# Optimization experiments

Measured on AMD Instinct MI355X. Metric: run time of the kernel, lower is better.

The kernel has to match this reference:

```python
import jax, jax.numpy as jnp
import numpy as np
from jax import lax

DIM = 256
QK = 256
HEADS = 8
NWIN = 7
TOPK = 4
KS = 5
SCALE = QK ** (-0.5)


def setup_inputs() -> dict:
    key = jax.random.key(0)
    ks = jax.random.split(key, 5)
    N, H, W = 8, 56, 56
    x = jax.random.normal(ks[0], (N, H, W, DIM), jnp.float32)
    W_qkv = jax.random.normal(ks[1], (DIM, QK + QK + DIM), jnp.float32) * 0.02
    b_qkv = jnp.zeros((QK + QK + DIM,), jnp.float32)
    lepe_w = jax.random.normal(ks[2], (DIM, 1, KS, KS), jnp.float32) * 0.05  # OIHW depthwise
    lepe_b = jnp.zeros((DIM,), jnp.float32)
    W_o = jax.random.normal(ks[3], (DIM, DIM), jnp.float32) * 0.02
    b_o = jnp.zeros((DIM,), jnp.float32)
    return {"x": x, "W_qkv": W_qkv, "b_qkv": b_qkv, "lepe_w": lepe_w,
            "lepe_b": lepe_b, "W_o": W_o, "b_o": b_o}


def reference(x, W_qkv, b_qkv, lepe_w, lepe_b, W_o, b_o):
    N, H, Wd, C = x.shape
    j = i = NWIN
    h, w = H // j, Wd // i
    p2, w2 = j * i, h * w
    hd, hdv = QK // HEADS, DIM // HEADS

    # window partition: n (j h) (i w) c -> n (j i) h w c
    xw = x.reshape(N, j, h, i, w, C).transpose(0, 1, 3, 2, 4, 5).reshape(N, p2, h, w, C)

    qkv = xw @ W_qkv + b_qkv                       # [N, p2, h, w, 2*QK+DIM... actually QK+(QK+DIM)]
    q = qkv[..., :QK]                              # [N, p2, h, w, QK]
    kv = qkv[..., QK:]                             # [N, p2, h, w, QK+DIM]

    q_pix = q.reshape(N, p2, w2, QK)
    kv_pix = kv.reshape(N, p2, w2, QK + DIM)       # identity kv_down

    q_win = q.mean(axis=(2, 3))                    # [N, p2, QK]
    k_win = kv[..., :QK].mean(axis=(2, 3))         # [N, p2, QK]

    # LePE: depthwise conv on v, in image layout
    v_img = kv[..., QK:].reshape(N, j, i, h, w, DIM).transpose(0, 5, 1, 3, 2, 4).reshape(N, DIM, H, Wd)
    pad = KS // 2
    lepe = lax.conv_general_dilated(v_img, lepe_w, (1, 1), [(pad, pad), (pad, pad)],
                                    feature_group_count=DIM)
    lepe = lepe + lepe_b[None, :, None, None]
    lepe = lepe.transpose(0, 2, 3, 1)              # [N, H, W, DIM]

    # coarse routing (detached in original when diff_routing=False)
    qd = lax.stop_gradient(q_win)
    kd = lax.stop_gradient(k_win)
    logit = jnp.einsum('npc,nqc->npq', qd * SCALE, kd)   # [N, p2, p2]
    _, r_idx = lax.top_k(logit, TOPK)              # [N, p2, TOPK]

    # gather top-k windows of kv (mul_weight='none')
    nidx = jnp.arange(N)[:, None, None]
    kv_sel = kv_pix[nidx, r_idx]                   # [N, p2, TOPK, w2, QK+DIM]
    k_sel = kv_sel[..., :QK].reshape(N, p2, TOPK * w2, HEADS, hd).transpose(0, 1, 3, 2, 4)
    v_sel = kv_sel[..., QK:].reshape(N, p2, TOPK * w2, HEADS, hdv).transpose(0, 1, 3, 2, 4)
    qh = q_pix.reshape(N, p2, w2, HEADS, hd).transpose(0, 1, 3, 2, 4)

    attn = jax.nn.softmax(jnp.einsum('npmwc,npmkc->npmwk', qh * SCALE, k_sel), axis=-1)
    out = jnp.einsum('npmwk,npmkc->npmwc', attn, v_sel)  # [N, p2, HEADS, w2, hdv]

    # back to image: (n p2) m (h w) c -> n (j h) (i w) (m c)
    out = out.transpose(0, 1, 3, 2, 4).reshape(N, j, i, h, w, DIM)
    out = out.transpose(0, 1, 3, 2, 4, 5).reshape(N, H, Wd, DIM)

    out = out + lepe
    out = out @ W_o + b_o
    return out
```

## Files before the change

### kernel.cpp

```cpp
#include <hip/hip_runtime.h>
#include <hip/hip_bf16.h>
#include <math.h>

#define NBATCH 8
#define HWDIM  56
#define NWIN   7
#define P2     49
#define HEADS  8
#define TOPK   4
#define SCALE  0.0625f
#define NPIX   (NBATCH*HWDIM*HWDIM)

typedef __attribute__((ext_vector_type(8))) short bf16x8;
typedef __attribute__((ext_vector_type(4))) float f32x4;

#define GLOBAL_AS __attribute__((address_space(1)))
#define LDS_AS    __attribute__((address_space(3)))

__device__ __forceinline__ void gload16(const unsigned short* g, unsigned short* l) {
  __builtin_amdgcn_global_load_lds((const GLOBAL_AS unsigned int*)g,
                                   (LDS_AS unsigned int*)l, 16, 0, 0);
}

__device__ __forceinline__ unsigned short f2bf(float f) {
  __hip_bfloat16 h = __float2bfloat16(f);
  return *reinterpret_cast<unsigned short*>(&h);
}
__device__ __forceinline__ float bf2f(unsigned short h) {
  return __uint_as_float(((unsigned)h) << 16);
}

__global__ __launch_bounds__(256) void conv_xwin(
    const float* __restrict__ x, unsigned short* __restrict__ xb,
    float* __restrict__ xw)
{
  __shared__ float4 red[256];
  const int bidx = blockIdx.x;
  const int n = bidx / P2, p = bidx - n * P2;
  const int y0 = (p / NWIN) * 8, x0 = (p % NWIN) * 8;
  const int t = threadIdx.x;
  const int c4 = t & 63, pg = t >> 6;
  float4 s = {0.f, 0.f, 0.f, 0.f};
  #pragma unroll
  for (int k = 0; k < 16; ++k) {
    const int pix = pg * 16 + k;
    const int yy = y0 + (pix >> 3), xx = x0 + (pix & 7);
    const size_t off = ((size_t)((n * HWDIM + yy) * HWDIM + xx)) * 256 + c4 * 4;
    float4 v = *(const float4*)&x[off];
    ushort4 o = { f2bf(v.x), f2bf(v.y), f2bf(v.z), f2bf(v.w) };
    *(ushort4*)&xb[off] = o;
    s.x += v.x; s.y += v.y; s.z += v.z; s.w += v.w;
  }
  red[t] = s;
  __syncthreads();
  if (pg == 0) {
    float4 a = red[c4], b = red[64 + c4], c = red[128 + c4], d = red[192 + c4];
    float4 o = { (a.x + b.x + c.x + d.x) * (1.f/64.f),
                 (a.y + b.y + c.y + d.y) * (1.f/64.f),
                 (a.z + b.z + c.z + d.z) * (1.f/64.f),
                 (a.w + b.w + c.w + d.w) * (1.f/64.f) };
    *(float4*)&xw[(size_t)bidx * 256 + c4 * 4] = o;
  }
}

__global__ __launch_bounds__(256) void prep_w(
    const float* __restrict__ W_qkv, const float* __restrict__ b_qkv,
    const float* __restrict__ W_o, const float* __restrict__ lepe_w,
    unsigned short* __restrict__ Wt_qkv, unsigned short* __restrict__ Wt_o,
    float* __restrict__ b_s, float* __restrict__ Wc)
{
  const int idx = blockIdx.x * 256 + threadIdx.x;
  if (idx < 768 * 256) {
    const int nn = idx >> 8, cc = idx & 255;
    float v = W_qkv[cc * 768 + nn];
    if (nn < 256) v *= SCALE;
    Wt_qkv[idx] = f2bf(v);
  } else if (idx < 768 * 256 + 256 * 256) {
    const int j = idx - 768 * 256;
    const int nn = j >> 8, cc = j & 255;
    Wt_o[j] = f2bf(W_o[cc * 256 + nn]);
  } else if (idx < 768 * 256 + 256 * 256 + 768) {
    const int j = idx - (768 * 256 + 256 * 256);
    b_s[j] = b_qkv[j] * (j < 256 ? SCALE : 1.f);
  } else if (idx < 768 * 256 + 256 * 256 + 768 + 25 * 256) {
    const int j = idx - (768 * 256 + 256 * 256 + 768);
    const int tap = j >> 8, cc = j & 255;
    Wc[j] = lepe_w[cc * 25 + tap];
  }
}

__global__ __launch_bounds__(256) void win_gemm(
    const float* __restrict__ xw, const float* __restrict__ W_qkv,
    const float* __restrict__ b_qkv,
    float* __restrict__ q_win, float* __restrict__ k_win)
{
  __shared__ float xs[256];
  const int bidx = blockIdx.x;
  const int t = threadIdx.x;
  xs[t] = xw[(size_t)bidx * 256 + t];
  __syncthreads();
  float aq = 0.f, ak = 0.f;
  for (int cc = 0; cc < 256; ++cc) {
    const float xv = xs[cc];
    aq = fmaf(xv, W_qkv[cc * 768 + t], aq);
    ak = fmaf(xv, W_qkv[cc * 768 + 256 + t], ak);
  }
  q_win[(size_t)bidx * 256 + t] = aq + b_qkv[t];
  k_win[(size_t)bidx * 256 + t] = ak + b_qkv[256 + t];
}

__global__ __launch_bounds__(256) void routing_topk(
    const float* __restrict__ q_win, const float* __restrict__ k_win,
    int* __restrict__ r_idx)
{
  __shared__ float qs[256];
  __shared__ float logit[64];
  const int bidx = blockIdx.x;
  const int n = bidx / P2;
  const int t = threadIdx.x;
  qs[t] = q_win[(size_t)bidx * 256 + t];
  __syncthreads();
  const int qq = t >> 2, qt = t & 3;
  if (qq < P2) {
    const float* kb = k_win + ((size_t)(n * P2 + qq)) * 256 + qt * 64;
    float a = 0.f;
    #pragma unroll 8
    for (int i = 0; i < 64; ++i) a = fmaf(qs[qt * 64 + i], kb[i], a);
    a += __shfl_xor(a, 1);
    a += __shfl_xor(a, 2);
    if (qt == 0) logit[qq] = a;
  }
  __syncthreads();
  if (t == 0) {
    float bv0 = -3e38f, bv1 = -3e38f, bv2 = -3e38f, bv3 = -3e38f;
    int bi0 = 0, bi1 = 0, bi2 = 0, bi3 = 0;
    for (int q2 = 0; q2 < P2; ++q2) {
      const float v = logit[q2];
      if (v > bv0) { bv3=bv2; bi3=bi2; bv2=bv1; bi2=bi1; bv1=bv0; bi1=bi0; bv0=v; bi0=q2; }
      else if (v > bv1) { bv3=bv2; bi3=bi2; bv2=bv1; bi2=bi1; bv1=v; bi1=q2; }
      else if (v > bv2) { bv3=bv2; bi3=bi2; bv2=v; bi2=q2; }
      else if (v > bv3) { bv3=v; bi3=q2; }
    }
    int* rp = r_idx + (size_t)bidx * TOPK;
    rp[0] = bi0; rp[1] = bi1; rp[2] = bi2; rp[3] = bi3;
  }
}

template<int MODE>
__global__ __launch_bounds__(512) void gemm_mfma(
    const unsigned short* __restrict__ A,
    const unsigned short* __restrict__ Bt,
    const float* __restrict__ bias,
    unsigned short* __restrict__ C0, unsigned short* __restrict__ C1,
    unsigned short* __restrict__ C2, float* __restrict__ Cf)
{
  __shared__ char smem[49152];
  unsigned short* Asm = (unsigned short*)smem;
  unsigned short* Bsm = (unsigned short*)(smem + 16384);
  float* Cs = (float*)smem;

  const int t = threadIdx.x;
  const int w = t >> 6, l = t & 63;
  const int wr = w >> 2, wc = w & 3;
  const int lr = l & 15, lg = l >> 4;
  const int bm = blockIdx.x, bn = blockIdx.y;
  const int row0 = bm * 128, col0 = bn * 256;

  const f32x4 fzero = {0.f, 0.f, 0.f, 0.f};
  f32x4 acc[4][4];
  #pragma unroll
  for (int m = 0; m < 4; ++m)
    #pragma unroll
    for (int n = 0; n < 4; ++n) acc[m][n] = fzero;

  const int srow  = t >> 3;
  const int skoff = ((t & 7) ^ (srow & 7)) * 8;

  for (int step = 0; step < 4; ++step) {
    const int k0 = step * 64;
    #pragma unroll
    for (int i = 0; i < 2; ++i)
      gload16(&A [(size_t)(row0 + i*64 + srow) * 256 + k0 + skoff],
              Asm + i*4096 + t*8);
    #pragma unroll
    for (int i = 0; i < 4; ++i)
      gload16(&Bt[(size_t)(col0 + i*64 + srow) * 256 + k0 + skoff],
              Bsm + i*4096 + t*8);
    __syncthreads();
    #pragma unroll
    for (int kk = 0; kk < 2; ++kk) {
      bf16x8 af[4], bb[4];
      #pragma unroll
      for (int m = 0; m < 4; ++m)
        af[m] = *(const bf16x8*)&Asm[(wr*64 + m*16 + lr) * 64 + ((kk*4 + lg) ^ (lr & 7)) * 8];
      #pragma unroll
      for (int n = 0; n < 4; ++n)
        bb[n] = *(const bf16x8*)&Bsm[(wc*64 + n*16 + lr) * 64 + ((kk*4 + lg) ^ (lr & 7)) * 8];
      #pragma unroll
      for (int m = 0; m < 4; ++m)
        #pragma unroll
        for (int n = 0; n < 4; ++n)
          acc[m][n] = __builtin_amdgcn_mfma_f32_16x16x32_bf16(af[m], bb[n], acc[m][n], 0, 0, 0);
    }
    __syncthreads();
  }

  float bcol[4];
  #pragma unroll
  for (int n = 0; n < 4; ++n) bcol[n] = bias[col0 + wc*64 + n*16 + lr];

  #pragma unroll
  for (int hf = 0; hf < 4; ++hf) {
    if (hf) __syncthreads();
    if (wr == (hf >> 1)) {
      const int mbase = (hf & 1) * 2;
      #pragma unroll
      for (int mm = 0; mm < 2; ++mm)
        #pragma unroll
        for (int n = 0; n < 4; ++n)
          #pragma unroll
          for (int r = 0; r < 4; ++r) {
            const int lrow = mm*16 + lg*4 + r;
            const int col  = wc*64 + n*16 + lr;
            const int csw  = col ^ ((lrow & 7) << 2);
            Cs[lrow * 256 + csw] = acc[mbase + mm][n][r] + bcol[n];
          }
    }
    __syncthreads();
    #pragma unroll
    for (int it = 0; it < 4; ++it) {
      const int d = (it * 512 + t) * 4;
      const int lrow = d >> 8;
      const int colL = (d & 255) ^ ((lrow & 7) << 2);
      f32x4 v = *(const f32x4*)&Cs[d];
      const size_t grow = (size_t)(row0 + hf*32 + lrow);
      if (MODE == 0) {
        unsigned short* Cp = (bn == 0) ? C0 : (bn == 1) ? C1 : C2;
        ushort4 o = { f2bf(v[0]), f2bf(v[1]), f2bf(v[2]), f2bf(v[3]) };
        *(ushort4*)&Cp[grow * 256 + colL] = o;
      } else {
        float4 o = { v[0], v[1], v[2], v[3] };
        *(float4*)&Cf[grow * 256 + colL] = o;
      }
    }
  }
}

#define PSTR 272

__global__ __launch_bounds__(256) void attn_mfma(
    const unsigned short* __restrict__ q_bf,
    const unsigned short* __restrict__ k_bf,
    const unsigned short* __restrict__ v_bf,
    const int* __restrict__ r_idx,
    unsigned short* __restrict__ o_bf)
{
  __shared__ char smem[52480];
  unsigned short* Ksm = (unsigned short*)smem;
  unsigned short* Qsm = (unsigned short*)(smem + 16384);
  unsigned short* Psm = (unsigned short*)smem;
  unsigned short* Vsm = (unsigned short*)(smem + 34816);
  float*          Osm = (float*)(smem + 34816);
  float*          Ls  = (float*)(smem + 52224);

  const int b = blockIdx.x;
  const int h = b & 7;
  const int np = b >> 3;
  const int n = np / P2, p = np - n * P2;
  const int t = threadIdx.x;
  const int w = t >> 6, l = t & 63;
  const int lr = l & 15, lg = l >> 4;

  const int4 rv = *(const int4*)&r_idx[np * 4];

  {
    const int pix = t >> 2, ch = t & 3;
    #pragma unroll
    for (int i = 0; i < 4; ++i) {
      const int wv = (&rv.x)[i];
      const int ky = (wv / NWIN) * 8 + (pix >> 3);
      const int kx = (wv % NWIN) * 8 + (pix & 7);
      const size_t goff = ((size_t)((n * HWDIM + ky) * HWDIM + kx)) * 256 + h * 32;
      gload16(&k_bf[goff + ch * 8], Ksm + i * 2048 + t * 8);
    }
    const int qy = (p / NWIN) * 8 + (pix >> 3);
    const int qx = (p % NWIN) * 8 + (pix & 7);
    gload16(&q_bf[((size_t)((n * HWDIM + qy) * HWDIM + qx)) * 256 + h * 32 + ch * 8],
            Qsm + t * 8);
  }
  {
    const int s = t >> 6, pix = t & 63;
    const int wv = (&rv.x)[s];
    const int ky = (wv / NWIN) * 8 + (pix >> 3);
    const int kx = (wv % NWIN) * 8 + (pix & 7);
    const size_t goff = ((size_t)((n * HWDIM + ky) * HWDIM + kx)) * 256 + h * 32;
    #pragma unroll
    for (int j = 0; j < 4; ++j) {
      bf16x8 vv = *(const bf16x8*)&v_bf[goff + j * 8];
      #pragma unroll
      for (int e = 0; e < 8; ++e)
        Vsm[(j * 8 + e) * PSTR + t] = (unsigned short)vv[e];
    }
  }
  __syncthreads();

  f32x4 sf[16];
  {
    const f32x4 fzero = {0.f, 0.f, 0.f, 0.f};
    bf16x8 aq = *(const bf16x8*)&Qsm[(w * 16 + lr) * 32 + lg * 8];
    #pragma unroll
    for (int f = 0; f < 16; ++f) {
      bf16x8 bk = *(const bf16x8*)&Ksm[(f * 16 + lr) * 32 + lg * 8];
      sf[f] = __builtin_amdgcn_mfma_f32_16x16x32_bf16(bk, aq, fzero, 0, 0, 0);
    }
  }

  {
    float mx = sf[0][0];
    #pragma unroll
    for (int f = 0; f < 16; ++f)
      #pragma unroll
      for (int r = 0; r < 4; ++r) mx = fmaxf(mx, sf[f][r]);
    mx = fmaxf(mx, __shfl_xor(mx, 16));
    mx = fmaxf(mx, __shfl_xor(mx, 32));
    float sum = 0.f;
    #pragma unroll
    for (int f = 0; f < 16; ++f)
      #pragma unroll
      for (int r = 0; r < 4; ++r) {
        float e = __expf(sf[f][r] - mx);
        sf[f][r] = e; sum += e;
      }
    sum += __shfl_xor(sum, 16);
    sum += __shfl_xor(sum, 32);
    if (lg == 0) Ls[w * 16 + lr] = 1.f / sum;
  }
  __syncthreads();

  #pragma unroll
  for (int f = 0; f < 16; ++f) {
    ushort4 pk = { f2bf(sf[f][0]), f2bf(sf[f][1]), f2bf(sf[f][2]), f2bf(sf[f][3]) };
    *(ushort4*)&Psm[(w * 16 + lr) * PSTR + f * 16 + lg * 4] = pk;
  }

  f32x4 oacc[2];
  oacc[0] = (f32x4){0.f, 0.f, 0.f, 0.f};
  oacc[1] = (f32x4){0.f, 0.f, 0.f, 0.f};
  #pragma unroll
  for (int ks = 0; ks < 8; ++ks) {
    bf16x8 ap = *(const bf16x8*)&Psm[(w * 16 + lr) * PSTR + ks * 32 + lg * 8];
    #pragma unroll
    for (int nn = 0; nn < 2; ++nn) {
      bf16x8 bv = *(const bf16x8*)&Vsm[(nn * 16 + lr) * PSTR + ks * 32 + lg * 8];
      oacc[nn] = __builtin_amdgcn_mfma_f32_16x16x32_bf16(ap, bv, oacc[nn], 0, 0, 0);
    }
  }

  float inv4[4];
  #pragma unroll
  for (int r = 0; r < 4; ++r) inv4[r] = Ls[w * 16 + lg * 4 + r];

  __syncthreads();
  #pragma unroll
  for (int nn = 0; nn < 2; ++nn)
    #pragma unroll
    for (int r = 0; r < 4; ++r)
      Osm[(w * 16 + lg * 4 + r) * 36 + nn * 16 + lr] = oacc[nn][r] * inv4[r];
  __syncthreads();
  {
    const int q = t >> 2, dq = (t & 3) * 8;
    const int qy = (p / NWIN) * 8 + (q >> 3);
    const int qx = (p % NWIN) * 8 + (q & 7);
    float vo[8];
    #pragma unroll
    for (int e = 0; e < 8; ++e) vo[e] = Osm[q * 36 + dq + e];
    ushort4 o0 = { f2bf(vo[0]), f2bf(vo[1]), f2bf(vo[2]), f2bf(vo[3]) };
    ushort4 o1 = { f2bf(vo[4]), f2bf(vo[5]), f2bf(vo[6]), f2bf(vo[7]) };
    unsigned short* op = &o_bf[((size_t)((n * HWDIM + qy) * HWDIM + qx)) * 256 + h * 32 + dq];
    *(ushort4*)op = o0;
    *(ushort4*)&op[4] = o1;
  }
}

__global__ __launch_bounds__(256) void lepe_add(
    const unsigned short* __restrict__ v_bf, const float* __restrict__ Wc,
    const float* __restrict__ bias, unsigned short* __restrict__ o_bf)
{
  const int gid = blockIdx.x * 256 + threadIdx.x;
  const int c8 = (gid & 31) * 8;
  const int pix = gid >> 5;
  const int n = pix / (HWDIM * HWDIM);
  const int rem = pix - n * (HWDIM * HWDIM);
  const int y = rem / HWDIM, x = rem - y * HWDIM;

  float acc[8];
  {
    float4 b0 = *(const float4*)&bias[c8];
    float4 b1 = *(const float4*)&bias[c8 + 4];
    acc[0]=b0.x; acc[1]=b0.y; acc[2]=b0.z; acc[3]=b0.w;
    acc[4]=b1.x; acc[5]=b1.y; acc[6]=b1.z; acc[7]=b1.w;
  }

  #pragma unroll
  for (int ky = 0; ky < 5; ++ky) {
    const int sy = y + ky - 2;
    if (sy < 0 || sy >= HWDIM) continue;
    #pragma unroll
    for (int kx = 0; kx < 5; ++kx) {
      const int sx = x + kx - 2;
      if (sx < 0 || sx >= HWDIM) continue;
      const bf16x8 vv = *(const bf16x8*)&v_bf[((size_t)((n * HWDIM + sy) * HWDIM + sx)) * 256 + c8];
      const float* wp = &Wc[(ky * 5 + kx) * 256 + c8];
      float4 w0 = *(const float4*)wp;
      float4 w1 = *(const float4*)(wp + 4);
      acc[0] = fmaf(w0.x, bf2f((unsigned short)vv[0]), acc[0]);
      acc[1] = fmaf(w0.y, bf2f((unsigned short)vv[1]), acc[1]);
      acc[2] = fmaf(w0.z, bf2f((unsigned short)vv[2]), acc[2]);
      acc[3] = fmaf(w0.w, bf2f((unsigned short)vv[3]), acc[3]);
      acc[4] = fmaf(w1.x, bf2f((unsigned short)vv[4]), acc[4]);
      acc[5] = fmaf(w1.y, bf2f((unsigned short)vv[5]), acc[5]);
      acc[6] = fmaf(w1.z, bf2f((unsigned short)vv[6]), acc[6]);
      acc[7] = fmaf(w1.w, bf2f((unsigned short)vv[7]), acc[7]);
    }
  }

  unsigned short* op = &o_bf[(size_t)pix * 256 + c8];
  const bf16x8 ov = *(const bf16x8*)op;
  ushort4 o0 = { f2bf(bf2f((unsigned short)ov[0]) + acc[0]),
                 f2bf(bf2f((unsigned short)ov[1]) + acc[1]),
                 f2bf(bf2f((unsigned short)ov[2]) + acc[2]),
                 f2bf(bf2f((unsigned short)ov[3]) + acc[3]) };
  ushort4 o1 = { f2bf(bf2f((unsigned short)ov[4]) + acc[4]),
                 f2bf(bf2f((unsigned short)ov[5]) + acc[5]),
                 f2bf(bf2f((unsigned short)ov[6]) + acc[6]),
                 f2bf(bf2f((unsigned short)ov[7]) + acc[7]) };
  *(ushort4*)op = o0;
  *(ushort4*)(op + 4) = o1;
}

extern "C" void kernel_launch(void* const* d_in, const int* in_sizes, int n_in,
                              void* d_out, int out_size, void* d_ws, size_t ws_size,
                              hipStream_t stream)
{
  const float* x      = (const float*)d_in[0];
  const float* W_qkv  = (const float*)d_in[1];
  const float* b_qkv  = (const float*)d_in[2];
  const float* lepe_w = (const float*)d_in[3];
  const float* lepe_b = (const float*)d_in[4];
  const float* W_o    = (const float*)d_in[5];
  const float* b_o    = (const float*)d_in[6];
  float* out = (float*)d_out;

  char* ws = (char*)d_ws;
  const size_t IMG = (size_t)NPIX * 256;
  unsigned short* x_bf    = (unsigned short*)(ws);
  unsigned short* q_bf    = (unsigned short*)(ws + 2*IMG);
  unsigned short* k_bf    = (unsigned short*)(ws + 4*IMG);
  unsigned short* v_bf    = (unsigned short*)(ws + 6*IMG);
  unsigned short* attn_bf = (unsigned short*)(ws + 8*IMG);
  unsigned short* Wt_qkv  = (unsigned short*)(ws + 10*IMG);
  unsigned short* Wt_o    = (unsigned short*)(ws + 10*IMG + 393216);
  float*          b_s     = (float*)         (ws + 10*IMG + 393216 + 131072);
  float*          x_win   = (float*)         (ws + 10*IMG + 393216 + 131072 + 4096);
  float*          q_win   = x_win + (size_t)NBATCH * P2 * 256;
  float*          k_win   = q_win + (size_t)NBATCH * P2 * 256;
  int*            ridx    = (int*)(k_win + (size_t)NBATCH * P2 * 256);
  float*          Wc      = (float*)(ridx + (size_t)NBATCH * P2 * TOPK);

  conv_xwin<<<NBATCH * P2, 256, 0, stream>>>(x, x_bf, x_win);
  prep_w<<<1052, 256, 0, stream>>>(W_qkv, b_qkv, W_o, lepe_w, Wt_qkv, Wt_o, b_s, Wc);
  win_gemm<<<NBATCH * P2, 256, 0, stream>>>(x_win, W_qkv, b_qkv, q_win, k_win);
  routing_topk<<<NBATCH * P2, 256, 0, stream>>>(q_win, k_win, ridx);
  gemm_mfma<0><<<dim3(196, 3), 512, 0, stream>>>(x_bf, Wt_qkv, b_s,
                                                 q_bf, k_bf, v_bf, nullptr);
  attn_mfma<<<NBATCH * P2 * HEADS, 256, 0, stream>>>(q_bf, k_bf, v_bf, ridx, attn_bf);
  lepe_add<<<3136, 256, 0, stream>>>(v_bf, Wc, lepe_b, attn_bf);
  gemm_mfma<1><<<dim3(196, 1), 512, 0, stream>>>(attn_bf, Wt_o, b_o,
                                                 nullptr, nullptr, nullptr, out);
}
```

Before: 217.4 us.

## Fuse preprocessing kernels, fold LePE conv into attention epilogue, add MFMA priority hints

Merges the bf16 conversion, window-mean, window q/k GEMM and weight-prep kernels into one launch with block-range dispatch. It also moves the depthwise LePE convolution into the attention kernel's epilogue, so the separate read-modify-write of the attention output is gone. s_setprio hints are wrapped around the MFMA loops in the GEMM and attention kernels. This removes launches and an extra pass over attn_bf, but makes the attention epilogue heavier with 25 strided v_bf loads per thread, which may hurt that kernel's occupancy or latency.

```diff
diff --git a/kernel.cpp b/kernel.cpp
--- a/kernel.cpp
+++ b/kernel.cpp
@@ -30,83 +30,74 @@
   return __uint_as_float(((unsigned)h) << 16);
 }
 
-__global__ __launch_bounds__(256) void conv_xwin(
-    const float* __restrict__ x, unsigned short* __restrict__ xb,
-    float* __restrict__ xw)
+__global__ __launch_bounds__(256) void fused_pre(
+    const float* __restrict__ x, const float* __restrict__ W_qkv,
+    const float* __restrict__ b_qkv, const float* __restrict__ W_o,
+    const float* __restrict__ lepe_w,
+    unsigned short* __restrict__ xb, float* __restrict__ q_win,
+    float* __restrict__ k_win, unsigned short* __restrict__ Wt_qkv,
+    unsigned short* __restrict__ Wt_o, float* __restrict__ b_s,
+    float* __restrict__ Wc)
 {
   __shared__ float4 red[256];
-  const int bidx = blockIdx.x;
-  const int n = bidx / P2, p = bidx - n * P2;
-  const int y0 = (p / NWIN) * 8, x0 = (p % NWIN) * 8;
-  const int t = threadIdx.x;
-  const int c4 = t & 63, pg = t >> 6;
-  float4 s = {0.f, 0.f, 0.f, 0.f};
-  #pragma unroll
-  for (int k = 0; k < 16; ++k) {
-    const int pix = pg * 16 + k;
-    const int yy = y0 + (pix >> 3), xx = x0 + (pix & 7);
-    const size_t off = ((size_t)((n * HWDIM + yy) * HWDIM + xx)) * 256 + c4 * 4;
-    float4 v = *(const float4*)&x[off];
-    ushort4 o = { f2bf(v.x), f2bf(v.y), f2bf(v.z), f2bf(v.w) };
-    *(ushort4*)&xb[off] = o;
-    s.x += v.x; s.y += v.y; s.z += v.z; s.w += v.w;
-  }
-  red[t] = s;
-  __syncthreads();
-  if (pg == 0) {
-    float4 a = red[c4], b = red[64 + c4], c = red[128 + c4], d = red[192 + c4];
-    float4 o = { (a.x + b.x + c.x + d.x) * (1.f/64.f),
-                 (a.y + b.y + c.y + d.y) * (1.f/64.f),
-                 (a.z + b.z + c.z + d.z) * (1.f/64.f),
-                 (a.w + b.w + c.w + d.w) * (1.f/64.f) };
-    *(float4*)&xw[(size_t)bidx * 256 + c4 * 4] = o;
-  }
-}
-
-__global__ __launch_bounds__(256) void prep_w(
-    const float* __restrict__ W_qkv, const float* __restrict__ b_qkv,
-    const float* __restrict__ W_o, const float* __restrict__ lepe_w,
-    unsigned short* __restrict__ Wt_qkv, unsigned short* __restrict__ Wt_o,
-    float* __restrict__ b_s, float* __restrict__ Wc)
-{
-  const int idx = blockIdx.x * 256 + threadIdx.x;
-  if (idx < 768 * 256) {
-    const int nn = idx >> 8, cc = idx & 255;
-    float v = W_qkv[cc * 768 + nn];
-    if (nn < 256) v *= SCALE;
-    Wt_qkv[idx] = f2bf(v);
-  } else if (idx < 768 * 256 + 256 * 256) {
-    const int j = idx - 768 * 256;
-    const int nn = j >> 8, cc = j & 255;
-    Wt_o[j] = f2bf(W_o[cc * 256 + nn]);
-  } else if (idx < 768 * 256 + 256 * 256 + 768) {
-    const int j = idx - (768 * 256 + 256 * 256);
-    b_s[j] = b_qkv[j] * (j < 256 ? SCALE : 1.f);
-  } else if (idx < 768 * 256 + 256 * 256 + 768 + 25 * 256) {
-    const int j = idx - (768 * 256 + 256 * 256 + 768);
-    const int tap = j >> 8, cc = j & 255;
-    Wc[j] = lepe_w[cc * 25 + tap];
-  }
-}
-
-__global__ __launch_bounds__(256) void win_gemm(
-    const float* __restrict__ xw, const float* __restrict__ W_qkv,
-    const float* __restrict__ b_qkv,
-    float* __restrict__ q_win, float* __restrict__ k_win)
-{
   __shared__ float xs[256];
   const int bidx = blockIdx.x;
   const int t = threadIdx.x;
-  xs[t] = xw[(size_t)bidx * 256 + t];
-  __syncthreads();
-  float aq = 0.f, ak = 0.f;
-  for (int cc = 0; cc < 256; ++cc) {
-    const float xv = xs[cc];
-    aq = fmaf(xv, W_qkv[cc * 768 + t], aq);
-    ak = fmaf(xv, W_qkv[cc * 768 + 256 + t], ak);
-  }
-  q_win[(size_t)bidx * 256 + t] = aq + b_qkv[t];
-  k_win[(size_t)bidx * 256 + t] = ak + b_qkv[256 + t];
+
+  if (bidx < NBATCH * P2) {
+    const int n = bidx / P2, p = bidx - n * P2;
+    const int y0 = (p / NWIN) * 8, x0 = (p % NWIN) * 8;
+    const int c4 = t & 63, pg = t >> 6;
+    float4 s = {0.f, 0.f, 0.f, 0.f};
+    #pragma unroll
+    for (int k = 0; k < 16; ++k) {
+      const int pix = pg * 16 + k;
+      const int yy = y0 + (pix >> 3), xx = x0 + (pix & 7);
+      const size_t off = ((size_t)((n * HWDIM + yy) * HWDIM + xx)) * 256 + c4 * 4;
+      float4 v = *(const float4*)&x[off];
+      ushort4 o = { f2bf(v.x), f2bf(v.y), f2bf(v.z), f2bf(v.w) };
+      *(ushort4*)&xb[off] = o;
+      s.x += v.x; s.y += v.y; s.z += v.z; s.w += v.w;
+    }
+    red[t] = s;
+    __syncthreads();
+    if (pg == 0) {
+      float4 a = red[c4], b = red[64 + c4], c = red[128 + c4], d = red[192 + c4];
+      float4 o = { (a.x + b.x + c.x + d.x) * (1.f/64.f),
+                   (a.y + b.y + c.y + d.y) * (1.f/64.f),
+                   (a.z + b.z + c.z + d.z) * (1.f/64.f),
+                   (a.w + b.w + c.w + d.w) * (1.f/64.f) };
+      *(float4*)&xs[c4 * 4] = o;
+    }
+    __syncthreads();
+    float aq = 0.f, ak = 0.f;
+    for (int cc = 0; cc < 256; ++cc) {
+      const float xv = xs[cc];
+      aq = fmaf(xv, W_qkv[cc * 768 + t], aq);
+      ak = fmaf(xv, W_qkv[cc * 768 + 256 + t], ak);
+    }
+    q_win[(size_t)bidx * 256 + t] = aq + b_qkv[t];
+    k_win[(size_t)bidx * 256 + t] = ak + b_qkv[256 + t];
+  } else {
+    const int idx = (bidx - NBATCH * P2) * 256 + t;
+    if (idx < 768 * 256) {
+      const int nn = idx >> 8, cc = idx & 255;
+      float v = W_qkv[cc * 768 + nn];
+      if (nn < 256) v *= SCALE;
+      Wt_qkv[idx] = f2bf(v);
+    } else if (idx < 768 * 256 + 256 * 256) {
+      const int j = idx - 768 * 256;
+      const int nn = j >> 8, cc = j & 255;
+      Wt_o[j] = f2bf(W_o[cc * 256 + nn]);
+    } else if (idx < 768 * 256 + 256 * 256 + 768) {
+      const int j = idx - (768 * 256 + 256 * 256);
+      b_s[j] = b_qkv[j] * (j < 256 ? SCALE : 1.f);
+    } else if (idx < 768 * 256 + 256 * 256 + 768 + 25 * 256) {
+      const int j = idx - (768 * 256 + 256 * 256 + 768);
+      const int tap = j >> 8, cc = j & 255;
+      Wc[j] = lepe_w[cc * 25 + tap];
+    }
+  }
 }
 
 __global__ __launch_bounds__(256) void routing_topk(
@@ -187,6 +178,7 @@
       gload16(&Bt[(size_t)(col0 + i*64 + srow) * 256 + k0 + skoff],
               Bsm + i*4096 + t*8);
     __syncthreads();
+    __builtin_amdgcn_s_setprio(1);
     #pragma unroll
     for (int kk = 0; kk < 2; ++kk) {
       bf16x8 af[4], bb[4];
@@ -202,6 +194,7 @@
         for (int n = 0; n < 4; ++n)
           acc[m][n] = __builtin_amdgcn_mfma_f32_16x16x32_bf16(af[m], bb[n], acc[m][n], 0, 0, 0);
     }
+    __builtin_amdgcn_s_setprio(0);
     __syncthreads();
   }
 
@@ -253,6 +246,8 @@
     const unsigned short* __restrict__ k_bf,
     const unsigned short* __restrict__ v_bf,
     const int* __restrict__ r_idx,
+    const float* __restrict__ Wc,
+    const float* __restrict__ lepe_b,
     unsigned short* __restrict__ o_bf)
 {
   __shared__ char smem[52480];
@@ -308,11 +303,13 @@
   {
     const f32x4 fzero = {0.f, 0.f, 0.f, 0.f};
     bf16x8 aq = *(const bf16x8*)&Qsm[(w * 16 + lr) * 32 + lg * 8];
+    __builtin_amdgcn_s_setprio(1);
     #pragma unroll
     for (int f = 0; f < 16; ++f) {
       bf16x8 bk = *(const bf16x8*)&Ksm[(f * 16 + lr) * 32 + lg * 8];
       sf[f] = __builtin_amdgcn_mfma_f32_16x16x32_bf16(bk, aq, fzero, 0, 0, 0);
     }
+    __builtin_amdgcn_s_setprio(0);
   }
 
   {
@@ -346,6 +343,7 @@
   f32x4 oacc[2];
   oacc[0] = (f32x4){0.f, 0.f, 0.f, 0.f};
   oacc[1] = (f32x4){0.f, 0.f, 0.f, 0.f};
+  __builtin_amdgcn_s_setprio(1);
   #pragma unroll
   for (int ks = 0; ks < 8; ++ks) {
     bf16x8 ap = *(const bf16x8*)&Psm[(w * 16 + lr) * PSTR + ks * 32 + lg * 8];
@@ -355,6 +353,7 @@
       oacc[nn] = __builtin_amdgcn_mfma_f32_16x16x32_bf16(ap, bv, oacc[nn], 0, 0, 0);
     }
   }
+  __builtin_amdgcn_s_setprio(0);
 
   float inv4[4];
   #pragma unroll
@@ -367,75 +366,51 @@
     for (int r = 0; r < 4; ++r)
       Osm[(w * 16 + lg * 4 + r) * 36 + nn * 16 + lr] = oacc[nn][r] * inv4[r];
   __syncthreads();
+
   {
     const int q = t >> 2, dq = (t & 3) * 8;
     const int qy = (p / NWIN) * 8 + (q >> 3);
     const int qx = (p % NWIN) * 8 + (q & 7);
+    const int c0 = h * 32 + dq;
+
+    float acc[8];
+    {
+      float4 b0 = *(const float4*)&lepe_b[c0];
+      float4 b1 = *(const float4*)&lepe_b[c0 + 4];
+      acc[0]=b0.x; acc[1]=b0.y; acc[2]=b0.z; acc[3]=b0.w;
+      acc[4]=b1.x; acc[5]=b1.y; acc[6]=b1.z; acc[7]=b1.w;
+    }
+    #pragma unroll
+    for (int ky = 0; ky < 5; ++ky) {
+      const int sy = qy + ky - 2;
+      if (sy < 0 || sy >= HWDIM) continue;
+      #pragma unroll
+      for (int kx = 0; kx < 5; ++kx) {
+        const int sx = qx + kx - 2;
+        if (sx < 0 || sx >= HWDIM) continue;
+        const bf16x8 vv = *(const bf16x8*)&v_bf[((size_t)((n * HWDIM + sy) * HWDIM + sx)) * 256 + c0];
+        const float* wp = &Wc[(ky * 5 + kx) * 256 + c0];
+        float4 w0 = *(const float4*)wp;
+        float4 w1 = *(const float4*)(wp + 4);
+        acc[0] = fmaf(w0.x, bf2f((unsigned short)vv[0]), acc[0]);
+        acc[1] = fmaf(w0.y, bf2f((unsigned short)vv[1]), acc[1]);
+        acc[2] = fmaf(w0.z, bf2f((unsigned short)vv[2]), acc[2]);
+        acc[3] = fmaf(w0.w, bf2f((unsigned short)vv[3]), acc[3]);
+        acc[4] = fmaf(w1.x, bf2f((unsigned short)vv[4]), acc[4]);
+        acc[5] = fmaf(w1.y, bf2f((unsigned short)vv[5]), acc[5]);
+        acc[6] = fmaf(w1.z, bf2f((unsigned short)vv[6]), acc[6]);
+        acc[7] = fmaf(w1.w, bf2f((unsigned short)vv[7]), acc[7]);
+      }
+    }
     float vo[8];
     #pragma unroll
-    for (int e = 0; e < 8; ++e) vo[e] = Osm[q * 36 + dq + e];
+    for (int e = 0; e < 8; ++e) vo[e] = Osm[q * 36 + dq + e] + acc[e];
     ushort4 o0 = { f2bf(vo[0]), f2bf(vo[1]), f2bf(vo[2]), f2bf(vo[3]) };
     ushort4 o1 = { f2bf(vo[4]), f2bf(vo[5]), f2bf(vo[6]), f2bf(vo[7]) };
-    unsigned short* op = &o_bf[((size_t)((n * HWDIM + qy) * HWDIM + qx)) * 256 + h * 32 + dq];
+    unsigned short* op = &o_bf[((size_t)((n * HWDIM + qy) * HWDIM + qx)) * 256 + c0];
     *(ushort4*)op = o0;
     *(ushort4*)&op[4] = o1;
   }
-}
-
-__global__ __launch_bounds__(256) void lepe_add(
-    const unsigned short* __restrict__ v_bf, const float* __restrict__ Wc,
-    const float* __restrict__ bias, unsigned short* __restrict__ o_bf)
-{
-  const int gid = blockIdx.x * 256 + threadIdx.x;
-  const int c8 = (gid & 31) * 8;
-  const int pix = gid >> 5;
-  const int n = pix / (HWDIM * HWDIM);
-  const int rem = pix - n * (HWDIM * HWDIM);
-  const int y = rem / HWDIM, x = rem - y * HWDIM;
-
-  float acc[8];
-  {
-    float4 b0 = *(const float4*)&bias[c8];
-    float4 b1 = *(const float4*)&bias[c8 + 4];
-    acc[0]=b0.x; acc[1]=b0.y; acc[2]=b0.z; acc[3]=b0.w;
-    acc[4]=b1.x; acc[5]=b1.y; acc[6]=b1.z; acc[7]=b1.w;
-  }
-
-  #pragma unroll
-  for (int ky = 0; ky < 5; ++ky) {
-    const int sy = y + ky - 2;
-    if (sy < 0 || sy >= HWDIM) continue;
-    #pragma unroll
-    for (int kx = 0; kx < 5; ++kx) {
-      const int sx = x + kx - 2;
-      if (sx < 0 || sx >= HWDIM) continue;
-      const bf16x8 vv = *(const bf16x8*)&v_bf[((size_t)((n * HWDIM + sy) * HWDIM + sx)) * 256 + c8];
-      const float* wp = &Wc[(ky * 5 + kx) * 256 + c8];
-      float4 w0 = *(const float4*)wp;
-      float4 w1 = *(const float4*)(wp + 4);
-      acc[0] = fmaf(w0.x, bf2f((unsigned short)vv[0]), acc[0]);
-      acc[1] = fmaf(w0.y, bf2f((unsigned short)vv[1]), acc[1]);
-      acc[2] = fmaf(w0.z, bf2f((unsigned short)vv[2]), acc[2]);
-      acc[3] = fmaf(w0.w, bf2f((unsigned short)vv[3]), acc[3]);
-      acc[4] = fmaf(w1.x, bf2f((unsigned short)vv[4]), acc[4]);
-      acc[5] = fmaf(w1.y, bf2f((unsigned short)vv[5]), acc[5]);
-      acc[6] = fmaf(w1.z, bf2f((unsigned short)vv[6]), acc[6]);
-      acc[7] = fmaf(w1.w, bf2f((unsigned short)vv[7]), acc[7]);
-    }
-  }
-
-  unsigned short* op = &o_bf[(size_t)pix * 256 + c8];
-  const bf16x8 ov = *(const bf16x8*)op;
-  ushort4 o0 = { f2bf(bf2f((unsigned short)ov[0]) + acc[0]),
-                 f2bf(bf2f((unsigned short)ov[1]) + acc[1]),
-                 f2bf(bf2f((unsigned short)ov[2]) + acc[2]),
-                 f2bf(bf2f((unsigned short)ov[3]) + acc[3]) };
-  ushort4 o1 = { f2bf(bf2f((unsigned short)ov[4]) + acc[4]),
-                 f2bf(bf2f((unsigned short)ov[5]) + acc[5]),
-                 f2bf(bf2f((unsigned short)ov[6]) + acc[6]),
-                 f2bf(bf2f((unsigned short)ov[7]) + acc[7]) };
-  *(ushort4*)op = o0;
-  *(ushort4*)(op + 4) = o1;
 }
 
 extern "C" void kernel_launch(void* const* d_in, const int* in_sizes, int n_in,
@@ -461,20 +436,18 @@
   unsigned short* Wt_qkv  = (unsigned short*)(ws + 10*IMG);
   unsigned short* Wt_o    = (unsigned short*)(ws + 10*IMG + 393216);
   float*          b_s     = (float*)         (ws + 10*IMG + 393216 + 131072);
-  float*          x_win   = (float*)         (ws + 10*IMG + 393216 + 131072 + 4096);
-  float*          q_win   = x_win + (size_t)NBATCH * P2 * 256;
+  float*          q_win   = (float*)         (ws + 10*IMG + 393216 + 131072 + 4096);
   float*          k_win   = q_win + (size_t)NBATCH * P2 * 256;
   int*            ridx    = (int*)(k_win + (size_t)NBATCH * P2 * 256);
   float*          Wc      = (float*)(ridx + (size_t)NBATCH * P2 * TOPK);
 
-  conv_xwin<<<NBATCH * P2, 256, 0, stream>>>(x, x_bf, x_win);
-  prep_w<<<1052, 256, 0, stream>>>(W_qkv, b_qkv, W_o, lepe_w, Wt_qkv, Wt_o, b_s, Wc);
-  win_gemm<<<NBATCH * P2, 256, 0, stream>>>(x_win, W_qkv, b_qkv, q_win, k_win);
+  fused_pre<<<NBATCH * P2 + 1052, 256, 0, stream>>>(
+      x, W_qkv, b_qkv, W_o, lepe_w, x_bf, q_win, k_win, Wt_qkv, Wt_o, b_s, Wc);
   routing_topk<<<NBATCH * P2, 256, 0, stream>>>(q_win, k_win, ridx);
   gemm_mfma<0><<<dim3(196, 3), 512, 0, stream>>>(x_bf, Wt_qkv, b_s,
                                                  q_bf, k_bf, v_bf, nullptr);
-  attn_mfma<<<NBATCH * P2 * HEADS, 256, 0, stream>>>(q_bf, k_bf, v_bf, ridx, attn_bf);
-  lepe_add<<<3136, 256, 0, stream>>>(v_bf, Wc, lepe_b, attn_bf);
+  attn_mfma<<<NBATCH * P2 * HEADS, 256, 0, stream>>>(q_bf, k_bf, v_bf, ridx,
+                                                     Wc, lepe_b, attn_bf);
   gemm_mfma<1><<<dim3(196, 1), 512, 0, stream>>>(attn_bf, Wt_o, b_o,
                                                  nullptr, nullptr, nullptr, out);
 }
```

Measured after the change: 213.6 us. No clear change (-1.8%).
